# Optimization experiments

Hardware: AMD Instinct MI355X
Metric: run time of the kernel (lower is better)

## Reference

```python
import jax, jax.numpy as jnp
import numpy as np

EPS = 2e-05
N_H_RDG = 9   # lifting scale grid: h_j = 2**j, j=0..8
N_H_CROP = 3  # group-conv scale support: offsets 0,1,2 (dyadic index shifts)


def _scaled_kernel(w, h):
    """Resample base kernel w [O, I, K] (taps on integers centered at 0) at
    coordinates x/h via linear interpolation -> [O, I, (K-1)*h+1], with the
    R+ Haar-measure normalization 1/h (psi_h(x) = psi(x/h)/h)."""
    K = w.shape[-1]
    Kh = (K - 1) * h + 1
    m = jnp.arange(K, dtype=jnp.float32) - K // 2
    x = (jnp.arange(Kh, dtype=jnp.float32) - Kh // 2) / h
    hat = jnp.maximum(0.0, 1.0 - jnp.abs(x[:, None] - m[None, :]))  # [Kh, K]
    return jnp.einsum('oim,xm->oix', w, hat) / h


def _conv1d_same(x, k):
    pad = (k.shape[-1] - 1) // 2
    return jax.lax.conv_general_dilated(
        x, k, window_strides=(1,), padding=[(pad, pad)],
        dimension_numbers=('NCH', 'OIH', 'NCH'))


def _pool_r1(x, stride):
    # max pool over the spatial (last) axis only: kernel 4, pad 1 each side
    return jax.lax.reduce_window(
        x, -jnp.inf, jax.lax.max,
        window_dimensions=(1, 1, 1, 4), window_strides=(1, 1, 1, stride),
        padding=((0, 0), (0, 0), (0, 0), (1, 1)))


def _bn(x, g, b):
    # BatchNorm2d over [B, C, H_scale, L], training-mode batch stats
    mu = jnp.mean(x, axis=(0, 2, 3), keepdims=True)
    var = jnp.var(x, axis=(0, 2, 3), keepdims=True)
    return (x - mu) * jax.lax.rsqrt(var + EPS) * g[None, :, None, None] + b[None, :, None, None]


def _forward(x, w1, w2, w3, g1, b1, g2, b2, g3, b3, fw1, fb1, fw2, fb2, fw3, fb3):
    B = x.shape[0]
    # --- c1: GConvRdG lifting, scales h_j = 2**j, j=0..8 ---
    out = jnp.stack([_conv1d_same(x, _scaled_kernel(w1, 2 ** j))
                     for j in range(N_H_RDG)], axis=2)      # [B,16,9,16]
    out = _bn(jax.nn.relu(_pool_r1(out, 2)), g1, b1)        # [B,16,9,8]
    # --- c2: GConvGG, h_crop=True: out scale j uses in scales j..j+2 ---
    O2, I2 = w2.shape[0], w2.shape[1]
    w2r = w2.reshape(O2, I2 * N_H_CROP, 3)
    H2 = out.shape[2] - (N_H_CROP - 1)  # 7
    out = jnp.stack([
        _conv1d_same(out[:, :, j:j + N_H_CROP, :].reshape(B, I2 * N_H_CROP, -1),
                     _scaled_kernel(w2r, 2 ** j))
        for j in range(H2)], axis=2)                        # [B,32,7,8]
    out = _bn(jax.nn.relu(_pool_r1(out, 2)), g2, b2)        # [B,32,7,4]
    # --- c3: GConvGG with 1x1 spatial kernel ---
    w3s = w3[:, :, :, 0]  # [64,32,3]
    H3 = out.shape[2] - (N_H_CROP - 1)  # 5
    out = jnp.stack([
        jnp.einsum('oik,bikl->bol', w3s, out[:, :, j:j + N_H_CROP, :]) / (2.0 ** j)
        for j in range(H3)], axis=2)                        # [B,64,5,4]
    out = _bn(jax.nn.relu(_pool_r1(out, 4)), g3, b3)        # [B,64,5,1]
    # --- MLP head (dropout is identity in eval) ---
    out = out.reshape(B, -1)                                # [B,320]
    out = out @ fw1.T + fb1
    out = out @ fw2.T + fb2
    return out @ fw3.T + fb3                                # [B,17]


def setup_inputs() -> dict:
    key = jax.random.key(0)
    ks = jax.random.split(key, 7)
    B = 4096
    x = jax.random.normal(ks[0], (B, 6, 16), dtype=jnp.float32)
    w1 = jax.random.normal(ks[1], (16, 6, 7), dtype=jnp.float32) * (6 * 7) ** -0.5
    w2 = jax.random.normal(ks[2], (32, 16, 3, 3), dtype=jnp.float32) * (16 * 3 * 3) ** -0.5
    w3 = jax.random.normal(ks[3], (64, 32, 3, 1), dtype=jnp.float32) * (32 * 3) ** -0.5
    fw1 = jax.random.normal(ks[4], (16, 320), dtype=jnp.float32) * 320 ** -0.5
    fw2 = jax.random.normal(ks[5], (16, 16), dtype=jnp.float32) * 16 ** -0.5
    fw3 = jax.random.normal(ks[6], (17, 16), dtype=jnp.float32) * 16 ** -0.5
    return {
        'x': x, 'w1': w1, 'w2': w2, 'w3': w3,
        'g1': jnp.ones(16), 'b1': jnp.zeros(16),
        'g2': jnp.ones(32), 'b2': jnp.zeros(32),
        'g3': jnp.ones(64), 'b3': jnp.zeros(64),
        'fw1': fw1, 'fb1': jnp.zeros(16),
        'fw2': fw2, 'fb2': jnp.zeros(16),
        'fw3': fw3, 'fb3': jnp.zeros(17),
    }


def reference(x, w1, w2, w3, g1, b1, g2, b2, g3, b3, fw1, fb1, fw2, fb2, fw3, fb3):
    return _forward(x, w1, w2, w3, g1, b1, g2, b2, g3, b3, fw1, fb1, fw2, fb2, fw3, fb3)
```

## Files before the change

kernel.cpp:

```cpp
#include <hip/hip_runtime.h>

#define EPS 2e-5f

using short8  = __attribute__((ext_vector_type(8))) short;
using floatx4 = __attribute__((ext_vector_type(4))) float;

static __device__ inline unsigned short f2bf(float f) {
    unsigned u = __float_as_uint(f);
    u += 0x7fffu + ((u >> 16) & 1u);
    return (unsigned short)(u >> 16);
}


__global__ void __launch_bounds__(256) k_setup(const float* __restrict__ w1,
                                               unsigned short* __restrict__ W1f,
                                               float* __restrict__ stats) {
    int gid = blockIdx.x * 256 + threadIdx.x;
    if (gid < 256) stats[gid] = 0.f;
    if (gid >= 221184) return;
    int j  = gid / 24576;
    int r  = gid % 24576;
    int T  = r / 1536;
    int r2 = r % 1536;
    int ks = r2 / 512;
    int r3 = r2 % 512;
    int lane = r3 >> 3, e = r3 & 7;
    int n  = T * 16 + (lane & 15);
    int kk = ks * 32 + (lane >> 4) * 8 + e;
    int o = n >> 4, t = n & 15;
    int i = kk >> 4, s = kk & 15;
    int h = 1 << j;
    int d = s - t;
    float val = 0.f;
    if (d >= -3 * h && d <= 3 * h) {
        float df = (float)d / (float)h;
        #pragma unroll
        for (int m = 0; m < 7; ++m) {
            float hat = fmaxf(0.f, 1.f - fabsf(df - (float)(m - 3)));
            val += w1[(o * 6 + i) * 7 + m] * hat;
        }
        val /= (float)h;
    }
    W1f[gid] = f2bf(val);
}

__global__ void __launch_bounds__(256) k1(const float* __restrict__ x,
                                          const unsigned short* __restrict__ W1f,
                                          unsigned short* __restrict__ p1,
                                          float* __restrict__ stats1) {
    int j    = blockIdx.y;
    int wav  = threadIdx.x >> 6;
    int lane = threadIdx.x & 63;
    int msub = wav & 1, nh = wav >> 1;
    int mt   = blockIdx.x * 2 + msub;
    int quad = lane >> 4, l15 = lane & 15;
    floatx4 z = {0.f, 0.f, 0.f, 0.f};
    floatx4 acc[8];
    #pragma unroll
    for (int T = 0; T < 8; ++T) acc[T] = z;
    const float* xr = x + (size_t)(mt * 16 + l15) * 96;
    const short8* Bj = (const short8*)W1f + (size_t)(j * 16) * 3 * 64;
    #pragma unroll
    for (int ks = 0; ks < 3; ++ks) {
        int k0 = ks * 32 + quad * 8;
        floatx4 v0 = *(const floatx4*)(xr + k0);
        floatx4 v1 = *(const floatx4*)(xr + k0 + 4);
        short8 a;
        #pragma unroll
        for (int e = 0; e < 4; ++e) {
            a[e]     = (short)f2bf(v0[e]);
            a[e + 4] = (short)f2bf(v1[e]);
        }
        #pragma unroll
        for (int T = 0; T < 8; ++T) {
            short8 b = Bj[((nh * 8 + T) * 3 + ks) * 64 + lane];
            acc[T] = __builtin_amdgcn_mfma_f32_16x16x32_bf16(a, b, acc[T], 0, 0, 0);
        }
    }
    __shared__ float ls[32];
    if (threadIdx.x < 32) ls[threadIdx.x] = 0.f;
    __syncthreads();
    int mbase = mt * 16 + quad * 4;
    int tp = l15;
    bool act = tp < 8;
    int tpe = tp & 7;
    int base = lane & 48;
    int c0 = base + max(2 * tpe - 1, 0);
    int c1 = base + 2 * tpe;
    int c2 = base + 2 * tpe + 1;
    int c3 = base + min(2 * tpe + 2, 15);
    #pragma unroll
    for (int T = 0; T < 8; ++T) {
        int o = nh * 8 + T;
        float psum = 0.f, pss = 0.f;
        #pragma unroll
        for (int r = 0; r < 4; ++r) {
            float v  = acc[T][r];
            float mx = fmaxf(fmaxf(__shfl(v, c0, 64), __shfl(v, c1, 64)),
                             fmaxf(__shfl(v, c2, 64), __shfl(v, c3, 64)));
            mx = fmaxf(mx, 0.f);
            if (act) {
                p1[(size_t)(mbase + r) * 1152 + o * 72 + j * 8 + tp] = f2bf(mx);
                psum += mx; pss += mx * mx;
            }
        }
        #pragma unroll
        for (int m = 32; m >= 1; m >>= 1) {
            psum += __shfl_xor(psum, m, 64);
            pss  += __shfl_xor(pss,  m, 64);
        }
        if (lane == 0) {
            atomicAdd(&ls[o], psum);
            atomicAdd(&ls[16 + o], pss);
        }
    }
    __syncthreads();
    if (threadIdx.x < 16) {
        atomicAdd(&stats1[threadIdx.x], ls[threadIdx.x]);
        atomicAdd(&stats1[16 + threadIdx.x], ls[16 + threadIdx.x]);
    }
}

__global__ void __launch_bounds__(384) k_bias(const float* __restrict__ w2,
                                              const float* __restrict__ g1,
                                              const float* __restrict__ b1,
                                              const float* __restrict__ stats1,
                                              unsigned short* __restrict__ W2f,
                                              float* __restrict__ bias2,
                                              float invN1) {
    int blk = blockIdx.x;
    int j   = blk >> 8;
    int col = blk & 255;
    int o = col >> 3, t = col & 7;
    int k = threadIdx.x;
    int ic = k >> 3, s = k & 7;
    int i = ic / 3, c = ic % 3;
    float mu  = stats1[i] * invN1;
    float var = stats1[16 + i] * invN1 - mu * mu;
    float rsg = rsqrtf(var + EPS);
    float a1  = g1[i] * rsg;
    float d1  = b1[i] - mu * a1;
    int h = 1 << j;
    int d = s - t;
    float raw = 0.f;
    if (d >= -h && d <= h) {
        float df = (float)d / (float)h;
        #pragma unroll
        for (int m = 0; m < 3; ++m) {
            float hat = fmaxf(0.f, 1.f - fabsf(df - (float)(m - 1)));
            raw += w2[((o * 16 + i) * 3 + c) * 3 + m] * hat;
        }
        raw /= (float)h;
    }
    {
        int T    = col >> 4;
        int lane = (col & 15) + ((k >> 3) & 3) * 16;
        int ks   = k >> 5;
        int e    = k & 7;
        W2f[(((size_t)(j * 16 + T) * 12 + ks) * 64 + lane) * 8 + e] = f2bf(raw * a1);
    }
    __shared__ float red[384];
    red[k] = raw * d1;
    __syncthreads();
    if (k < 128) red[k] += red[k + 128] + red[k + 256];
    __syncthreads();
    for (int st = 64; st >= 1; st >>= 1) {
        if (k < st) red[k] += red[k + st];
        __syncthreads();
    }
    if (k == 0) bias2[j * 256 + col] = red[0];
}

__global__ void __launch_bounds__(256) k2(const unsigned short* __restrict__ p1,
                                          const unsigned short* __restrict__ W2f,
                                          const float* __restrict__ bias2,
                                          unsigned short* __restrict__ p2s,
                                          float* __restrict__ stats2,
                                          int B) {
    int j    = blockIdx.y;
    int wav  = threadIdx.x >> 6;
    int lane = threadIdx.x & 63;
    int nh   = wav & 1, mp = wav >> 1;
    int m0   = blockIdx.x * 64 + mp * 32;
    int quad = lane >> 4, l15 = lane & 15;
    floatx4 z = {0.f, 0.f, 0.f, 0.f};
    floatx4 acc[2][8];
    #pragma unroll
    for (int mi = 0; mi < 2; ++mi)
        #pragma unroll
        for (int T = 0; T < 8; ++T) acc[mi][T] = z;
    const short8* Bj = (const short8*)W2f + (size_t)(j * 16) * 12 * 64;
    const unsigned short* Arow0 = p1 + (size_t)(m0 + l15) * 1152;
    const unsigned short* Arow1 = Arow0 + 16 * 1152;
    #pragma unroll
    for (int ks = 0; ks < 12; ++ks) {
        int k0 = ks * 32 + quad * 8;
        int i  = k0 / 24;
        int c  = (k0 - i * 24) >> 3;
        int off = i * 72 + (j + c) * 8;
        short8 a0 = *(const short8*)(Arow0 + off);
        short8 a1 = *(const short8*)(Arow1 + off);
        #pragma unroll
        for (int T = 0; T < 8; ++T) {
            short8 b = Bj[((nh * 8 + T) * 12 + ks) * 64 + lane];
            acc[0][T] = __builtin_amdgcn_mfma_f32_16x16x32_bf16(a0, b, acc[0][T], 0, 0, 0);
            acc[1][T] = __builtin_amdgcn_mfma_f32_16x16x32_bf16(a1, b, acc[1][T], 0, 0, 0);
        }
    }
    __shared__ float ls[64];
    if (threadIdx.x < 64) ls[threadIdx.x] = 0.f;
    __syncthreads();
    int tp  = lane & 7;
    bool act = tp < 4;
    int tpe = tp & 3;
    int base = lane & 56;
    int c0 = base + max(2 * tpe - 1, 0);
    int c1 = base + 2 * tpe;
    int c2 = base + 2 * tpe + 1;
    int c3 = base + min(2 * tpe + 2, 7);
    #pragma unroll
    for (int T = 0; T < 8; ++T) {
        int n = (nh * 8 + T) * 16 + l15;
        int o = n >> 3;
        float bias = bias2[j * 256 + n];
        float psum = 0.f, pss = 0.f;
        #pragma unroll
        for (int mi = 0; mi < 2; ++mi) {
            int mbase = m0 + mi * 16 + quad * 4;
            #pragma unroll
            for (int r = 0; r < 4; ++r) {
                float v  = acc[mi][T][r] + bias;
                float mx = fmaxf(fmaxf(__shfl(v, c0, 64), __shfl(v, c1, 64)),
                                 fmaxf(__shfl(v, c2, 64), __shfl(v, c3, 64)));
                mx = fmaxf(mx, 0.f);
                if (act) {
                    p2s[(((size_t)j * 4 + tp) * B + mbase + r) * 32 + o] = f2bf(mx);
                    psum += mx; pss += mx * mx;
                }
            }
        }
        #pragma unroll
        for (int m = 0; m < 5; ++m) {
            int msk = (m < 3) ? (1 << m) : (1 << (m + 1));
            psum += __shfl_xor(psum, msk, 64);
            pss  += __shfl_xor(pss,  msk, 64);
        }
        if (lane == 0 || lane == 8) {
            int oo = (nh * 8 + T) * 2 + (lane >> 3);
            atomicAdd(&ls[oo], psum);
            atomicAdd(&ls[32 + oo], pss);
        }
    }
    __syncthreads();
    if (threadIdx.x < 32) {
        atomicAdd(&stats2[threadIdx.x], ls[threadIdx.x]);
        atomicAdd(&stats2[32 + threadIdx.x], ls[32 + threadIdx.x]);
    }
}

__global__ void __launch_bounds__(256) k3(const unsigned short* __restrict__ p2s,
                                          const float* __restrict__ w3,
                                          const float* __restrict__ g2,
                                          const float* __restrict__ b2,
                                          const float* __restrict__ stats2,
                                          float* __restrict__ act3,
                                          float* __restrict__ stats3,
                                          float invN2, int B) {
    int j    = blockIdx.y;
    int wav  = threadIdx.x >> 6;
    int lane = threadIdx.x & 63;
    int msub = wav & 1, nh = wav >> 1;
    int m0   = (blockIdx.x * 2 + msub) * 16;
    int quad = lane >> 4, l15 = lane & 15;
    __shared__ float a2s[32], d2s[32], bias3s[64], ls[128];
    __shared__ unsigned short W3s[6144];
    if (threadIdx.x < 128) ls[threadIdx.x] = 0.f;
    if (threadIdx.x < 32) {
        int i = threadIdx.x;
        float mu  = stats2[i] * invN2;
        float var = stats2[32 + i] * invN2 - mu * mu;
        float rsg = rsqrtf(var + EPS);
        a2s[i] = g2[i] * rsg;
        d2s[i] = b2[i] - mu * a2s[i];
    }
    __syncthreads();
    for (int idx = threadIdx.x; idx < 6144; idx += 256) {
        int e  = idx & 7;
        int ln = (idx >> 3) & 63;
        int fs = idx >> 9;
        int Tg = fs / 3, ks = fs % 3;
        int n = Tg * 16 + (ln & 15);
        int i = (ln >> 4) * 8 + e;
        W3s[idx] = f2bf(w3[n * 96 + i * 3 + ks] * a2s[i]);
    }
    if (threadIdx.x < 64) {
        float s = 0.f;
        for (int i = 0; i < 32; ++i)
            #pragma unroll
            for (int kk = 0; kk < 3; ++kk)
                s = fmaf(w3[threadIdx.x * 96 + i * 3 + kk], d2s[i], s);
        bias3s[threadIdx.x] = s;
    }
    __syncthreads();
    short8 bf[2][3];
    #pragma unroll
    for (int T = 0; T < 2; ++T)
        #pragma unroll
        for (int ks = 0; ks < 3; ++ks)
            bf[T][ks] = *(const short8*)&W3s[(((nh * 2 + T) * 3 + ks) * 64 + lane) * 8];
    floatx4 z = {0.f, 0.f, 0.f, 0.f};
    floatx4 acc[2][3];
    #pragma unroll
    for (int T = 0; T < 2; ++T)
        #pragma unroll
        for (int l = 0; l < 3; ++l) acc[T][l] = z;
    #pragma unroll
    for (int ks = 0; ks < 3; ++ks) {
        int jj = j + ks;
        #pragma unroll
        for (int l = 0; l < 3; ++l) {
            const short8* ap =
                (const short8*)(p2s + ((size_t)(jj * 4 + l) * B + m0 + l15) * 32) + quad;
            short8 a = *ap;
            #pragma unroll
            for (int T = 0; T < 2; ++T)
                acc[T][l] = __builtin_amdgcn_mfma_f32_16x16x32_bf16(a, bf[T][ks],
                                                                    acc[T][l], 0, 0, 0);
        }
    }
    float inv = 1.f / (float)(1 << j);
    int mbase = m0 + quad * 4;
    #pragma unroll
    for (int T = 0; T < 2; ++T) {
        int col = nh * 32 + T * 16 + l15;
        float bias = bias3s[col];
        float psum = 0.f, pss = 0.f;
        #pragma unroll
        for (int r = 0; r < 4; ++r) {
            float v = fmaxf(fmaxf(acc[T][0][r], acc[T][1][r]), acc[T][2][r]);
            v = fmaxf((v + bias) * inv, 0.f);
            act3[(size_t)(mbase + r) * 320 + col * 5 + j] = v;
            psum += v; pss += v * v;
        }
        psum += __shfl_xor(psum, 16, 64); pss += __shfl_xor(pss, 16, 64);
        psum += __shfl_xor(psum, 32, 64); pss += __shfl_xor(pss, 32, 64);
        if (quad == 0) {
            atomicAdd(&ls[col], psum);
            atomicAdd(&ls[64 + col], pss);
        }
    }
    __syncthreads();
    if (threadIdx.x < 64) {
        atomicAdd(&stats3[threadIdx.x], ls[threadIdx.x]);
        atomicAdd(&stats3[64 + threadIdx.x], ls[64 + threadIdx.x]);
    }
}

__global__ void __launch_bounds__(128) k4(const float* __restrict__ act3,
                                          const float* __restrict__ g3,
                                          const float* __restrict__ b3,
                                          const float* __restrict__ stats3,
                                          const float* __restrict__ fw1,
                                          const float* __restrict__ fb1,
                                          const float* __restrict__ fw2,
                                          const float* __restrict__ fb2,
                                          const float* __restrict__ fw3,
                                          const float* __restrict__ fb3,
                                          float* __restrict__ out,
                                          float invN3) {
    __shared__ float a3s[64], d3s[64];
    __shared__ unsigned short W1s[5120];
    __shared__ float fw2s[256], fw3s[272], fb2s[16], fb3s[17], fb1f[16];
    __shared__ float hbuf[2][16][17];
    int tid = threadIdx.x;
    if (tid < 64) {
        float mu  = stats3[tid] * invN3;
        float var = stats3[64 + tid] * invN3 - mu * mu;
        float rsg = rsqrtf(var + EPS);
        a3s[tid] = g3[tid] * rsg;
        d3s[tid] = b3[tid] - mu * a3s[tid];
    }
    __syncthreads();
    for (int idx = tid; idx < 5120; idx += 128) {
        int e  = idx & 7;
        int ln = (idx >> 3) & 63;
        int ks = idx >> 9;
        int n  = ln & 15;
        int k  = ks * 32 + (ln >> 4) * 8 + e;
        W1s[idx] = f2bf(fw1[n * 320 + k] * a3s[k / 5]);
    }
    for (int idx = tid; idx < 256; idx += 128) fw2s[idx] = fw2[idx];
    for (int idx = tid; idx < 272; idx += 128) fw3s[idx] = fw3[idx];
    if (tid < 16) fb2s[tid] = fb2[tid];
    if (tid < 17) fb3s[tid] = fb3[tid];
    if (tid < 16) {
        float s = fb1[tid];
        for (int o = 0; o < 64; ++o) {
            float dd = d3s[o];
            #pragma unroll
            for (int jj = 0; jj < 5; ++jj)
                s = fmaf(fw1[tid * 320 + o * 5 + jj], dd, s);
        }
        fb1f[tid] = s;
    }
    __syncthreads();
    int wav = tid >> 6, lane = tid & 63;
    int quad = lane >> 4, l15 = lane & 15;
    int mt = blockIdx.x * 2 + wav;
    const float* ar = act3 + (size_t)(mt * 16 + l15) * 320;
    floatx4 acc = {0.f, 0.f, 0.f, 0.f};
    #pragma unroll
    for (int ks = 0; ks < 10; ++ks) {
        int k0 = ks * 32 + quad * 8;
        floatx4 v0 = *(const floatx4*)(ar + k0);
        floatx4 v1 = *(const floatx4*)(ar + k0 + 4);
        short8 a;
        #pragma unroll
        for (int e = 0; e < 4; ++e) {
            a[e]     = (short)f2bf(v0[e]);
            a[e + 4] = (short)f2bf(v1[e]);
        }
        short8 b = *(const short8*)&W1s[(ks * 64 + lane) * 8];
        acc = __builtin_amdgcn_mfma_f32_16x16x32_bf16(a, b, acc, 0, 0, 0);
    }
    #pragma unroll
    for (int r = 0; r < 4; ++r)
        hbuf[wav][quad * 4 + r][l15] = acc[r] + fb1f[l15];
    __syncthreads();
    if (lane < 16) {
        int row = l15;
        float hv[16];
        #pragma unroll
        for (int n = 0; n < 16; ++n) hv[n] = hbuf[wav][row][n];
        float h2[16];
        #pragma unroll
        for (int f2 = 0; f2 < 16; ++f2) {
            float s = fb2s[f2];
            #pragma unroll
            for (int n = 0; n < 16; ++n) s = fmaf(fw2s[f2 * 16 + n], hv[n], s);
            h2[f2] = s;
        }
        float* orow = out + (size_t)(mt * 16 + row) * 17;
        #pragma unroll
        for (int f3 = 0; f3 < 17; ++f3) {
            float s = fb3s[f3];
            #pragma unroll
            for (int n = 0; n < 16; ++n) s = fmaf(fw3s[f3 * 16 + n], h2[n], s);
            orow[f3] = s;
        }
    }
}

extern "C" void kernel_launch(void* const* d_in, const int* in_sizes, int n_in,
                              void* d_out, int out_size, void* d_ws, size_t ws_size,
                              hipStream_t stream) {
    (void)n_in; (void)out_size; (void)ws_size;
    const float* x   = (const float*)d_in[0];
    const float* w1  = (const float*)d_in[1];
    const float* w2  = (const float*)d_in[2];
    const float* w3  = (const float*)d_in[3];
    const float* g1  = (const float*)d_in[4];
    const float* b1  = (const float*)d_in[5];
    const float* g2  = (const float*)d_in[6];
    const float* b2  = (const float*)d_in[7];
    const float* g3  = (const float*)d_in[8];
    const float* b3  = (const float*)d_in[9];
    const float* fw1 = (const float*)d_in[10];
    const float* fb1 = (const float*)d_in[11];
    const float* fw2 = (const float*)d_in[12];
    const float* fb2 = (const float*)d_in[13];
    const float* fw3 = (const float*)d_in[14];
    const float* fb3 = (const float*)d_in[15];
    float* out = (float*)d_out;

    int B = in_sizes[0] / 96;

    char* wsb = (char*)d_ws;
    float*          stats  = (float*)wsb;
    unsigned short* W1f    = (unsigned short*)(wsb + 1024);
    unsigned short* W2f    = W1f + 221184;
    float*          bias2  = (float*)(W2f + 688128);
    unsigned short* p1     = (unsigned short*)(bias2 + 1792);
    unsigned short* p2s    = p1 + (size_t)B * 1152;
    float*          act3   = (float*)(p2s + (size_t)B * 896);

    float* stats1 = stats;
    float* stats2 = stats + 32;
    float* stats3 = stats + 96;

    float invN1 = 1.f / (float)(B * 72);
    float invN2 = 1.f / (float)(B * 28);
    float invN3 = 1.f / (float)(B * 5);

    k_setup<<<864, 256, 0, stream>>>(w1, W1f, stats);
    k1<<<dim3(B / 32, 9), 256, 0, stream>>>(x, W1f, p1, stats1);
    k_bias<<<7 * 256, 384, 0, stream>>>(w2, g1, b1, stats1, W2f, bias2, invN1);
    k2<<<dim3(B / 64, 7), 256, 0, stream>>>(p1, W2f, bias2, p2s, stats2, B);
    k3<<<dim3(B / 32, 5), 256, 0, stream>>>(p2s, w3, g2, b2, stats2, act3, stats3,
                                            invN2, B);
    k4<<<B / 32, 128, 0, stream>>>(act3, g3, b3, stats3, fw1, fb1, fw2, fb2, fw3, fb3,
                                   out, invN3);
}
```

Baseline: 204.1 us.

## Fuse weight prep into conv kernels, use per-block stat partials and bf16 activations

Removes the separate weight-setup and bias kernels: each conv kernel now builds its scaled bf16 weight fragments in registers from the raw weights and folds the BN affine of the previous layer in-kernel. Global atomics for batch statistics are replaced by per-block partial sums reduced by the consumer kernel. Intermediate layouts are changed to scale-major and act3 is stored as bf16, and grids are made persistent-ish with fixed block counts looping over tiles. This cuts kernel launches, workspace traffic and atomic contention, at the cost of redundant weight recomputation per block and a smaller, hardcoded grid (e.g. 32 blocks in x) that ties work split to B=4096.

```diff
diff --git a/kernel.cpp b/kernel.cpp
--- a/kernel.cpp
+++ b/kernel.cpp
@@ -3,6 +3,7 @@
 #define EPS 2e-5f
 
 using short8  = __attribute__((ext_vector_type(8))) short;
+using short4v = __attribute__((ext_vector_type(4))) short;
 using floatx4 = __attribute__((ext_vector_type(4))) float;
 
 static __device__ inline unsigned short f2bf(float f) {
@@ -12,75 +13,49 @@
 }
 
 
-__global__ void __launch_bounds__(256) k_setup(const float* __restrict__ w1,
-                                               unsigned short* __restrict__ W1f,
-                                               float* __restrict__ stats) {
-    int gid = blockIdx.x * 256 + threadIdx.x;
-    if (gid < 256) stats[gid] = 0.f;
-    if (gid >= 221184) return;
-    int j  = gid / 24576;
-    int r  = gid % 24576;
-    int T  = r / 1536;
-    int r2 = r % 1536;
-    int ks = r2 / 512;
-    int r3 = r2 % 512;
-    int lane = r3 >> 3, e = r3 & 7;
-    int n  = T * 16 + (lane & 15);
-    int kk = ks * 32 + (lane >> 4) * 8 + e;
-    int o = n >> 4, t = n & 15;
-    int i = kk >> 4, s = kk & 15;
+__global__ void __launch_bounds__(256) k1(const float* __restrict__ x,
+                                          const float* __restrict__ w1,
+                                          unsigned short* __restrict__ p1,
+                                          float* __restrict__ partials1,
+                                          int B) {
+    __shared__ float w1s[672];
+    __shared__ float ls[32];
+    __shared__ unsigned short ptile[32][16][8];
+    int tid = threadIdx.x, j = blockIdx.y;
+    int wav = tid >> 6, lane = tid & 63;
+    int quad = lane >> 4, l15 = lane & 15;
+    int msub = wav & 1, nh = wav >> 1;
+    for (int idx = tid; idx < 672; idx += 256) w1s[idx] = w1[idx];
+    if (tid < 32) ls[tid] = 0.f;
+    __syncthreads();
     int h = 1 << j;
-    int d = s - t;
-    float val = 0.f;
-    if (d >= -3 * h && d <= 3 * h) {
-        float df = (float)d / (float)h;
-        #pragma unroll
-        for (int m = 0; m < 7; ++m) {
-            float hat = fmaxf(0.f, 1.f - fabsf(df - (float)(m - 3)));
-            val += w1[(o * 6 + i) * 7 + m] * hat;
-        }
-        val /= (float)h;
-    }
-    W1f[gid] = f2bf(val);
-}
-
-__global__ void __launch_bounds__(256) k1(const float* __restrict__ x,
-                                          const unsigned short* __restrict__ W1f,
-                                          unsigned short* __restrict__ p1,
-                                          float* __restrict__ stats1) {
-    int j    = blockIdx.y;
-    int wav  = threadIdx.x >> 6;
-    int lane = threadIdx.x & 63;
-    int msub = wav & 1, nh = wav >> 1;
-    int mt   = blockIdx.x * 2 + msub;
-    int quad = lane >> 4, l15 = lane & 15;
-    floatx4 z = {0.f, 0.f, 0.f, 0.f};
-    floatx4 acc[8];
-    #pragma unroll
-    for (int T = 0; T < 8; ++T) acc[T] = z;
-    const float* xr = x + (size_t)(mt * 16 + l15) * 96;
-    const short8* Bj = (const short8*)W1f + (size_t)(j * 16) * 3 * 64;
-    #pragma unroll
-    for (int ks = 0; ks < 3; ++ks) {
-        int k0 = ks * 32 + quad * 8;
-        floatx4 v0 = *(const floatx4*)(xr + k0);
-        floatx4 v1 = *(const floatx4*)(xr + k0 + 4);
-        short8 a;
-        #pragma unroll
-        for (int e = 0; e < 4; ++e) {
-            a[e]     = (short)f2bf(v0[e]);
-            a[e + 4] = (short)f2bf(v1[e]);
-        }
-        #pragma unroll
-        for (int T = 0; T < 8; ++T) {
-            short8 b = Bj[((nh * 8 + T) * 3 + ks) * 64 + lane];
-            acc[T] = __builtin_amdgcn_mfma_f32_16x16x32_bf16(a, b, acc[T], 0, 0, 0);
-        }
-    }
-    __shared__ float ls[32];
-    if (threadIdx.x < 32) ls[threadIdx.x] = 0.f;
-    __syncthreads();
-    int mbase = mt * 16 + quad * 4;
+    float hInv = 1.f / (float)h;
+    short8 bf[8][3];
+    #pragma unroll
+    for (int T = 0; T < 8; ++T) {
+        int o = nh * 8 + T;
+        #pragma unroll
+        for (int ks = 0; ks < 3; ++ks) {
+            short8 v;
+            #pragma unroll
+            for (int e = 0; e < 8; ++e) {
+                int k = ks * 32 + quad * 8 + e;
+                int i = k >> 4, s = k & 15;
+                int d = s - l15;
+                float val = 0.f;
+                if (d >= -3 * h && d <= 3 * h) {
+                    float u = (float)d * hInv + 3.f;
+                    int m0 = (int)u;
+                    float f = u - (float)m0;
+                    int m1 = min(m0 + 1, 6);
+                    const float* wr = &w1s[(o * 6 + i) * 7];
+                    val = (wr[m0] * (1.f - f) + wr[m1] * f) * hInv;
+                }
+                v[e] = (short)f2bf(val);
+            }
+            bf[T][ks] = v;
+        }
+    }
     int tp = l15;
     bool act = tp < 8;
     int tpe = tp & 7;
@@ -89,277 +64,317 @@
     int c1 = base + 2 * tpe;
     int c2 = base + 2 * tpe + 1;
     int c3 = base + min(2 * tpe + 2, 15);
-    #pragma unroll
-    for (int T = 0; T < 8; ++T) {
-        int o = nh * 8 + T;
-        float psum = 0.f, pss = 0.f;
-        #pragma unroll
-        for (int r = 0; r < 4; ++r) {
-            float v  = acc[T][r];
-            float mx = fmaxf(fmaxf(__shfl(v, c0, 64), __shfl(v, c1, 64)),
-                             fmaxf(__shfl(v, c2, 64), __shfl(v, c3, 64)));
-            mx = fmaxf(mx, 0.f);
-            if (act) {
-                p1[(size_t)(mbase + r) * 1152 + o * 72 + j * 8 + tp] = f2bf(mx);
-                psum += mx; pss += mx * mx;
-            }
-        }
-        #pragma unroll
-        for (int m = 32; m >= 1; m >>= 1) {
-            psum += __shfl_xor(psum, m, 64);
-            pss  += __shfl_xor(pss,  m, 64);
-        }
-        if (lane == 0) {
-            atomicAdd(&ls[o], psum);
-            atomicAdd(&ls[16 + o], pss);
-        }
-    }
-    __syncthreads();
-    if (threadIdx.x < 16) {
-        atomicAdd(&stats1[threadIdx.x], ls[threadIdx.x]);
-        atomicAdd(&stats1[16 + threadIdx.x], ls[16 + threadIdx.x]);
-    }
-}
-
-__global__ void __launch_bounds__(384) k_bias(const float* __restrict__ w2,
-                                              const float* __restrict__ g1,
-                                              const float* __restrict__ b1,
-                                              const float* __restrict__ stats1,
-                                              unsigned short* __restrict__ W2f,
-                                              float* __restrict__ bias2,
-                                              float invN1) {
-    int blk = blockIdx.x;
-    int j   = blk >> 8;
-    int col = blk & 255;
-    int o = col >> 3, t = col & 7;
-    int k = threadIdx.x;
-    int ic = k >> 3, s = k & 7;
-    int i = ic / 3, c = ic % 3;
-    float mu  = stats1[i] * invN1;
-    float var = stats1[16 + i] * invN1 - mu * mu;
-    float rsg = rsqrtf(var + EPS);
-    float a1  = g1[i] * rsg;
-    float d1  = b1[i] - mu * a1;
-    int h = 1 << j;
-    int d = s - t;
-    float raw = 0.f;
-    if (d >= -h && d <= h) {
-        float df = (float)d / (float)h;
-        #pragma unroll
-        for (int m = 0; m < 3; ++m) {
-            float hat = fmaxf(0.f, 1.f - fabsf(df - (float)(m - 1)));
-            raw += w2[((o * 16 + i) * 3 + c) * 3 + m] * hat;
-        }
-        raw /= (float)h;
-    }
-    {
-        int T    = col >> 4;
-        int lane = (col & 15) + ((k >> 3) & 3) * 16;
-        int ks   = k >> 5;
-        int e    = k & 7;
-        W2f[(((size_t)(j * 16 + T) * 12 + ks) * 64 + lane) * 8 + e] = f2bf(raw * a1);
-    }
-    __shared__ float red[384];
-    red[k] = raw * d1;
-    __syncthreads();
-    if (k < 128) red[k] += red[k + 128] + red[k + 256];
-    __syncthreads();
-    for (int st = 64; st >= 1; st >>= 1) {
-        if (k < st) red[k] += red[k + st];
+    for (int it = 0; it < 4; ++it) {
+        int t32 = blockIdx.x * 4 + it;
+        int mt  = t32 * 2 + msub;
+        floatx4 z = {0.f, 0.f, 0.f, 0.f};
+        floatx4 acc[8];
+        #pragma unroll
+        for (int T = 0; T < 8; ++T) acc[T] = z;
+        const float* xr = x + (size_t)(mt * 16 + l15) * 96;
+        #pragma unroll
+        for (int ks = 0; ks < 3; ++ks) {
+            int k0 = ks * 32 + quad * 8;
+            floatx4 v0 = *(const floatx4*)(xr + k0);
+            floatx4 v1 = *(const floatx4*)(xr + k0 + 4);
+            short8 a;
+            #pragma unroll
+            for (int e = 0; e < 4; ++e) {
+                a[e]     = (short)f2bf(v0[e]);
+                a[e + 4] = (short)f2bf(v1[e]);
+            }
+            #pragma unroll
+            for (int T = 0; T < 8; ++T)
+                acc[T] = __builtin_amdgcn_mfma_f32_16x16x32_bf16(a, bf[T][ks], acc[T], 0, 0, 0);
+        }
         __syncthreads();
-    }
-    if (k == 0) bias2[j * 256 + col] = red[0];
-}
-
-__global__ void __launch_bounds__(256) k2(const unsigned short* __restrict__ p1,
-                                          const unsigned short* __restrict__ W2f,
-                                          const float* __restrict__ bias2,
-                                          unsigned short* __restrict__ p2s,
-                                          float* __restrict__ stats2,
-                                          int B) {
-    int j    = blockIdx.y;
-    int wav  = threadIdx.x >> 6;
-    int lane = threadIdx.x & 63;
-    int nh   = wav & 1, mp = wav >> 1;
-    int m0   = blockIdx.x * 64 + mp * 32;
-    int quad = lane >> 4, l15 = lane & 15;
-    floatx4 z = {0.f, 0.f, 0.f, 0.f};
-    floatx4 acc[2][8];
-    #pragma unroll
-    for (int mi = 0; mi < 2; ++mi)
-        #pragma unroll
-        for (int T = 0; T < 8; ++T) acc[mi][T] = z;
-    const short8* Bj = (const short8*)W2f + (size_t)(j * 16) * 12 * 64;
-    const unsigned short* Arow0 = p1 + (size_t)(m0 + l15) * 1152;
-    const unsigned short* Arow1 = Arow0 + 16 * 1152;
-    #pragma unroll
-    for (int ks = 0; ks < 12; ++ks) {
-        int k0 = ks * 32 + quad * 8;
-        int i  = k0 / 24;
-        int c  = (k0 - i * 24) >> 3;
-        int off = i * 72 + (j + c) * 8;
-        short8 a0 = *(const short8*)(Arow0 + off);
-        short8 a1 = *(const short8*)(Arow1 + off);
+        int row_l = msub * 16 + quad * 4;
         #pragma unroll
         for (int T = 0; T < 8; ++T) {
-            short8 b = Bj[((nh * 8 + T) * 12 + ks) * 64 + lane];
-            acc[0][T] = __builtin_amdgcn_mfma_f32_16x16x32_bf16(a0, b, acc[0][T], 0, 0, 0);
-            acc[1][T] = __builtin_amdgcn_mfma_f32_16x16x32_bf16(a1, b, acc[1][T], 0, 0, 0);
-        }
-    }
-    __shared__ float ls[64];
-    if (threadIdx.x < 64) ls[threadIdx.x] = 0.f;
-    __syncthreads();
-    int tp  = lane & 7;
-    bool act = tp < 4;
-    int tpe = tp & 3;
-    int base = lane & 56;
-    int c0 = base + max(2 * tpe - 1, 0);
-    int c1 = base + 2 * tpe;
-    int c2 = base + 2 * tpe + 1;
-    int c3 = base + min(2 * tpe + 2, 7);
-    #pragma unroll
-    for (int T = 0; T < 8; ++T) {
-        int n = (nh * 8 + T) * 16 + l15;
-        int o = n >> 3;
-        float bias = bias2[j * 256 + n];
-        float psum = 0.f, pss = 0.f;
-        #pragma unroll
-        for (int mi = 0; mi < 2; ++mi) {
-            int mbase = m0 + mi * 16 + quad * 4;
+            int o = nh * 8 + T;
+            float psum = 0.f, pss = 0.f;
             #pragma unroll
             for (int r = 0; r < 4; ++r) {
-                float v  = acc[mi][T][r] + bias;
+                float v  = acc[T][r];
                 float mx = fmaxf(fmaxf(__shfl(v, c0, 64), __shfl(v, c1, 64)),
                                  fmaxf(__shfl(v, c2, 64), __shfl(v, c3, 64)));
                 mx = fmaxf(mx, 0.f);
                 if (act) {
-                    p2s[(((size_t)j * 4 + tp) * B + mbase + r) * 32 + o] = f2bf(mx);
+                    ptile[row_l + r][o][tp] = f2bf(mx);
                     psum += mx; pss += mx * mx;
                 }
             }
-        }
-        #pragma unroll
-        for (int m = 0; m < 5; ++m) {
-            int msk = (m < 3) ? (1 << m) : (1 << (m + 1));
-            psum += __shfl_xor(psum, msk, 64);
-            pss  += __shfl_xor(pss,  msk, 64);
-        }
-        if (lane == 0 || lane == 8) {
-            int oo = (nh * 8 + T) * 2 + (lane >> 3);
-            atomicAdd(&ls[oo], psum);
-            atomicAdd(&ls[32 + oo], pss);
-        }
-    }
-    __syncthreads();
-    if (threadIdx.x < 32) {
-        atomicAdd(&stats2[threadIdx.x], ls[threadIdx.x]);
-        atomicAdd(&stats2[32 + threadIdx.x], ls[32 + threadIdx.x]);
-    }
+            #pragma unroll
+            for (int m = 32; m >= 1; m >>= 1) {
+                psum += __shfl_xor(psum, m, 64);
+                pss  += __shfl_xor(pss,  m, 64);
+            }
+            if (lane == 0) {
+                atomicAdd(&ls[o], psum);
+                atomicAdd(&ls[16 + o], pss);
+            }
+        }
+        __syncthreads();
+        unsigned short* dst = p1 + ((size_t)j * B + t32 * 32) * 128;
+        #pragma unroll
+        for (int u = 0; u < 2; ++u) {
+            int c = tid + u * 256;
+            int rr = c >> 4, oo = c & 15;
+            *(short8*)(dst + (size_t)rr * 128 + oo * 8) = *(const short8*)&ptile[rr][oo][0];
+        }
+    }
+    __syncthreads();
+    if (tid < 32) partials1[(size_t)(blockIdx.y * 32 + blockIdx.x) * 32 + tid] = ls[tid];
+}
+
+__global__ void __launch_bounds__(256) k2(const unsigned short* __restrict__ p1,
+                                          const float* __restrict__ w2,
+                                          const float* __restrict__ g1,
+                                          const float* __restrict__ b1,
+                                          const float* __restrict__ partials1,
+                                          unsigned short* __restrict__ p2s,
+                                          float* __restrict__ partials2,
+                                          int B) {
+    __shared__ float w2s[4608];
+    __shared__ float red[8][32];
+    __shared__ float st1[32];
+    __shared__ float a1s[16], d1s[16];
+    __shared__ float wt[4][2][16][17];
+    __shared__ float wbias[4][16];
+    __shared__ unsigned short pt[4 * 32 * 8];
+    __shared__ float ls2[64];
+    int tid = threadIdx.x;
+    int w = tid >> 6, lane = tid & 63;
+    int quad = lane >> 4, l15 = lane & 15;
+    int j = blockIdx.z, cs = blockIdx.y;
+    float invN1 = 1.f / (float)(B * 72);
+    for (int idx = tid; idx < 4608; idx += 256) w2s[idx] = w2[idx];
+    {
+        int ch = tid & 31, grp = tid >> 5;
+        float s = 0.f;
+        for (int g = grp; g < 288; g += 8) s += partials1[(size_t)g * 32 + ch];
+        red[grp][ch] = s;
+    }
+    if (tid < 64) ls2[tid] = 0.f;
+    __syncthreads();
+    if (tid < 32) {
+        float s = 0.f;
+        #pragma unroll
+        for (int g = 0; g < 8; ++g) s += red[g][tid];
+        st1[tid] = s;
+    }
+    __syncthreads();
+    if (tid < 16) {
+        float mu  = st1[tid] * invN1;
+        float var = st1[16 + tid] * invN1 - mu * mu;
+        float rs  = rsqrtf(var + EPS);
+        a1s[tid] = g1[tid] * rs;
+        d1s[tid] = b1[tid] - mu * a1s[tid];
+    }
+    __syncthreads();
+    int h = 1 << j;
+    float hInv = 1.f / (float)h;
+    int n = cs * 64 + w * 16 + l15;
+    int o = n >> 3, t = n & 7;
+    float biasacc = 0.f;
+    short8 af[12];
+    #pragma unroll
+    for (int ks = 0; ks < 12; ++ks) {
+        int ic = ks * 4 + quad;
+        int i = ic / 3, c = ic - i * 3;
+        const float* wr = &w2s[((o * 16 + i) * 3 + c) * 3];
+        short8 v;
+        #pragma unroll
+        for (int e = 0; e < 8; ++e) {
+            int d = e - t;
+            float raw = 0.f;
+            if (d >= -h && d <= h) {
+                float u = (float)d * hInv + 1.f;
+                int m0 = (int)u;
+                float f = u - (float)m0;
+                int m1 = min(m0 + 1, 2);
+                raw = (wr[m0] * (1.f - f) + wr[m1] * f) * hInv;
+            }
+            v[e] = (short)f2bf(raw * a1s[i]);
+            biasacc = fmaf(raw, d1s[i], biasacc);
+        }
+        af[ks] = v;
+    }
+    biasacc += __shfl_xor(biasacc, 16, 64);
+    biasacc += __shfl_xor(biasacc, 32, 64);
+    if (quad == 0) wbias[w][l15] = biasacc;
+    __syncthreads();
+    float ps[2] = {0.f, 0.f}, pq[2] = {0.f, 0.f};
+    int lo = max(0, 2 * quad - 1), hi = min(7, 2 * quad + 2);
+    for (int it = 0; it < 8; ++it) {
+        int b0 = (blockIdx.x * 16 + it * 2) * 16;
+        floatx4 accA = {0.f, 0.f, 0.f, 0.f};
+        floatx4 accB = {0.f, 0.f, 0.f, 0.f};
+        #pragma unroll
+        for (int ks = 0; ks < 12; ++ks) {
+            int ic = ks * 4 + quad;
+            int i = ic / 3, c = ic - i * 3;
+            const unsigned short* pr = p1 + ((size_t)(j + c) * B + b0 + l15) * 128 + i * 8;
+            short8 bA = *(const short8*)pr;
+            short8 bB = *(const short8*)(pr + 16 * 128);
+            accA = __builtin_amdgcn_mfma_f32_16x16x32_bf16(af[ks], bA, accA, 0, 0, 0);
+            accB = __builtin_amdgcn_mfma_f32_16x16x32_bf16(af[ks], bB, accB, 0, 0, 0);
+        }
+        __syncthreads();
+        #pragma unroll
+        for (int r = 0; r < 4; ++r) {
+            float br = wbias[w][quad * 4 + r];
+            wt[w][0][quad * 4 + r][l15] = accA[r] + br;
+            wt[w][1][quad * 4 + r][l15] = accB[r] + br;
+        }
+        __syncthreads();
+        #pragma unroll
+        for (int s_ = 0; s_ < 2; ++s_)
+            #pragma unroll
+            for (int u = 0; u < 2; ++u) {
+                float m = -1e30f;
+                for (int t_ = lo; t_ <= hi; ++t_) m = fmaxf(m, wt[w][s_][u * 8 + t_][l15]);
+                float v = fmaxf(m, 0.f);
+                pt[(quad * 32 + s_ * 16 + l15) * 8 + w * 2 + u] = f2bf(v);
+                ps[u] += v; pq[u] += v * v;
+            }
+        __syncthreads();
+        {
+            int tpp = tid >> 6, rem = tid & 63;
+            int bL = rem >> 1, og = rem & 1;
+            *(short4v*)(p2s + ((size_t)(j * 4 + tpp) * B + b0 + bL) * 32 + cs * 8 + og * 4) =
+                *(const short4v*)&pt[(tpp * 32 + bL) * 8 + og * 4];
+        }
+    }
+    #pragma unroll
+    for (int m = 1; m <= 32; m <<= 1) {
+        #pragma unroll
+        for (int u = 0; u < 2; ++u) {
+            ps[u] += __shfl_xor(ps[u], m, 64);
+            pq[u] += __shfl_xor(pq[u], m, 64);
+        }
+    }
+    if (lane == 0) {
+        int o0 = cs * 8 + w * 2;
+        #pragma unroll
+        for (int u = 0; u < 2; ++u) {
+            ls2[(o0 + u) * 2]     = ps[u];
+            ls2[(o0 + u) * 2 + 1] = pq[u];
+        }
+    }
+    __syncthreads();
+    int bid = blockIdx.x + 16 * (cs + 4 * j);
+    if (tid < 64) partials2[(size_t)bid * 64 + tid] = ls2[tid];
 }
 
 __global__ void __launch_bounds__(256) k3(const unsigned short* __restrict__ p2s,
                                           const float* __restrict__ w3,
                                           const float* __restrict__ g2,
                                           const float* __restrict__ b2,
-                                          const float* __restrict__ stats2,
-                                          float* __restrict__ act3,
-                                          float* __restrict__ stats3,
-                                          float invN2, int B) {
-    int j    = blockIdx.y;
-    int wav  = threadIdx.x >> 6;
-    int lane = threadIdx.x & 63;
-    int msub = wav & 1, nh = wav >> 1;
-    int m0   = (blockIdx.x * 2 + msub) * 16;
+                                          const float* __restrict__ partials2,
+                                          unsigned short* __restrict__ act3,
+                                          float* __restrict__ partials3,
+                                          int B) {
+    __shared__ float w3s[6144];
+    __shared__ float red[4][64];
+    __shared__ float st2[64];
+    __shared__ float a2s[32], d2s[32];
+    __shared__ float ls3[128];
+    int tid = threadIdx.x;
+    int wav = tid >> 6, lane = tid & 63;
     int quad = lane >> 4, l15 = lane & 15;
-    __shared__ float a2s[32], d2s[32], bias3s[64], ls[128];
-    __shared__ unsigned short W3s[6144];
-    if (threadIdx.x < 128) ls[threadIdx.x] = 0.f;
-    if (threadIdx.x < 32) {
-        int i = threadIdx.x;
-        float mu  = stats2[i] * invN2;
-        float var = stats2[32 + i] * invN2 - mu * mu;
-        float rsg = rsqrtf(var + EPS);
-        a2s[i] = g2[i] * rsg;
-        d2s[i] = b2[i] - mu * a2s[i];
-    }
-    __syncthreads();
-    for (int idx = threadIdx.x; idx < 6144; idx += 256) {
-        int e  = idx & 7;
-        int ln = (idx >> 3) & 63;
-        int fs = idx >> 9;
-        int Tg = fs / 3, ks = fs % 3;
-        int n = Tg * 16 + (ln & 15);
-        int i = (ln >> 4) * 8 + e;
-        W3s[idx] = f2bf(w3[n * 96 + i * 3 + ks] * a2s[i]);
-    }
-    if (threadIdx.x < 64) {
+    int j = blockIdx.y;
+    float invN2 = 1.f / (float)(B * 28);
+    for (int idx = tid; idx < 6144; idx += 256) w3s[idx] = w3[idx];
+    {
+        int ch = tid & 63, grp = tid >> 6;
         float s = 0.f;
-        for (int i = 0; i < 32; ++i)
-            #pragma unroll
-            for (int kk = 0; kk < 3; ++kk)
-                s = fmaf(w3[threadIdx.x * 96 + i * 3 + kk], d2s[i], s);
-        bias3s[threadIdx.x] = s;
-    }
-    __syncthreads();
-    short8 bf[2][3];
-    #pragma unroll
-    for (int T = 0; T < 2; ++T)
-        #pragma unroll
-        for (int ks = 0; ks < 3; ++ks)
-            bf[T][ks] = *(const short8*)&W3s[(((nh * 2 + T) * 3 + ks) * 64 + lane) * 8];
-    floatx4 z = {0.f, 0.f, 0.f, 0.f};
-    floatx4 acc[2][3];
-    #pragma unroll
-    for (int T = 0; T < 2; ++T)
-        #pragma unroll
-        for (int l = 0; l < 3; ++l) acc[T][l] = z;
-    #pragma unroll
-    for (int ks = 0; ks < 3; ++ks) {
-        int jj = j + ks;
-        #pragma unroll
-        for (int l = 0; l < 3; ++l) {
-            const short8* ap =
-                (const short8*)(p2s + ((size_t)(jj * 4 + l) * B + m0 + l15) * 32) + quad;
-            short8 a = *ap;
-            #pragma unroll
-            for (int T = 0; T < 2; ++T)
-                acc[T][l] = __builtin_amdgcn_mfma_f32_16x16x32_bf16(a, bf[T][ks],
-                                                                    acc[T][l], 0, 0, 0);
-        }
-    }
+        for (int g = grp; g < 448; g += 4) s += partials2[(size_t)g * 64 + ch];
+        red[grp][ch] = s;
+    }
+    __syncthreads();
+    if (tid < 64) st2[tid] = red[0][tid] + red[1][tid] + red[2][tid] + red[3][tid];
+    __syncthreads();
+    if (tid < 32) {
+        float mu  = st2[tid * 2] * invN2;
+        float var = st2[tid * 2 + 1] * invN2 - mu * mu;
+        float rs  = rsqrtf(var + EPS);
+        a2s[tid] = g2[tid] * rs;
+        d2s[tid] = b2[tid] - mu * a2s[tid];
+    }
+    __syncthreads();
+    int og = wav;
+    int o  = og * 16 + l15;
+    float biasacc = 0.f;
+    short8 af[3];
+    #pragma unroll
+    for (int kf = 0; kf < 3; ++kf) {
+        short8 v;
+        #pragma unroll
+        for (int e = 0; e < 8; ++e) {
+            int i = quad * 8 + e;
+            float raw = w3s[o * 96 + i * 3 + kf];
+            v[e] = (short)f2bf(raw * a2s[i]);
+            biasacc = fmaf(raw, d2s[i], biasacc);
+        }
+        af[kf] = v;
+    }
+    biasacc += __shfl_xor(biasacc, 16, 64);
+    biasacc += __shfl_xor(biasacc, 32, 64);
+    float brow[4];
+    #pragma unroll
+    for (int r = 0; r < 4; ++r) brow[r] = __shfl(biasacc, quad * 4 + r, 64);
     float inv = 1.f / (float)(1 << j);
-    int mbase = m0 + quad * 4;
-    #pragma unroll
-    for (int T = 0; T < 2; ++T) {
-        int col = nh * 32 + T * 16 + l15;
-        float bias = bias3s[col];
-        float psum = 0.f, pss = 0.f;
+    float ps[4] = {0.f, 0.f, 0.f, 0.f}, pq[4] = {0.f, 0.f, 0.f, 0.f};
+    for (int it = 0; it < 8; ++it) {
+        int b0 = (blockIdx.x * 8 + it) * 16;
+        floatx4 aL0 = {0.f, 0.f, 0.f, 0.f};
+        floatx4 aL1 = {0.f, 0.f, 0.f, 0.f};
+        floatx4 aL2 = {0.f, 0.f, 0.f, 0.f};
+        #pragma unroll
+        for (int c = 0; c < 3; ++c) {
+            const unsigned short* prb = p2s + ((size_t)(j + c) * 4 * B + b0 + l15) * 32 + quad * 8;
+            short8 b0f = *(const short8*)prb;
+            short8 b1f = *(const short8*)(prb + (size_t)B * 32);
+            short8 b2f = *(const short8*)(prb + (size_t)2 * B * 32);
+            aL0 = __builtin_amdgcn_mfma_f32_16x16x32_bf16(af[c], b0f, aL0, 0, 0, 0);
+            aL1 = __builtin_amdgcn_mfma_f32_16x16x32_bf16(af[c], b1f, aL1, 0, 0, 0);
+            aL2 = __builtin_amdgcn_mfma_f32_16x16x32_bf16(af[c], b2f, aL2, 0, 0, 0);
+        }
+        short4v pk;
         #pragma unroll
         for (int r = 0; r < 4; ++r) {
-            float v = fmaxf(fmaxf(acc[T][0][r], acc[T][1][r]), acc[T][2][r]);
-            v = fmaxf((v + bias) * inv, 0.f);
-            act3[(size_t)(mbase + r) * 320 + col * 5 + j] = v;
-            psum += v; pss += v * v;
-        }
-        psum += __shfl_xor(psum, 16, 64); pss += __shfl_xor(pss, 16, 64);
-        psum += __shfl_xor(psum, 32, 64); pss += __shfl_xor(pss, 32, 64);
-        if (quad == 0) {
-            atomicAdd(&ls[col], psum);
-            atomicAdd(&ls[64 + col], pss);
-        }
-    }
-    __syncthreads();
-    if (threadIdx.x < 64) {
-        atomicAdd(&stats3[threadIdx.x], ls[threadIdx.x]);
-        atomicAdd(&stats3[64 + threadIdx.x], ls[64 + threadIdx.x]);
-    }
+            float vm = fmaxf(fmaxf(aL0[r], aL1[r]), aL2[r]);
+            float v  = fmaxf((vm + brow[r]) * inv, 0.f);
+            pk[r] = (short)f2bf(v);
+            ps[r] += v; pq[r] += v * v;
+        }
+        *(short4v*)(act3 + ((size_t)j * B + b0 + l15) * 64 + og * 16 + quad * 4) = pk;
+    }
+    #pragma unroll
+    for (int m = 1; m <= 8; m <<= 1) {
+        #pragma unroll
+        for (int r = 0; r < 4; ++r) {
+            ps[r] += __shfl_xor(ps[r], m, 64);
+            pq[r] += __shfl_xor(pq[r], m, 64);
+        }
+    }
+    if (l15 == 0) {
+        #pragma unroll
+        for (int r = 0; r < 4; ++r) {
+            ls3[(og * 16 + quad * 4 + r) * 2]     = ps[r];
+            ls3[(og * 16 + quad * 4 + r) * 2 + 1] = pq[r];
+        }
+    }
+    __syncthreads();
+    int bid = blockIdx.x + 32 * j;
+    if (tid < 128) partials3[(size_t)bid * 128 + tid] = ls3[tid];
 }
 
-__global__ void __launch_bounds__(128) k4(const float* __restrict__ act3,
+__global__ void __launch_bounds__(256) k4(const unsigned short* __restrict__ act3,
                                           const float* __restrict__ g3,
                                           const float* __restrict__ b3,
-                                          const float* __restrict__ stats3,
+                                          const float* __restrict__ partials3,
                                           const float* __restrict__ fw1,
                                           const float* __restrict__ fb1,
                                           const float* __restrict__ fw2,
@@ -367,62 +382,70 @@
                                           const float* __restrict__ fw3,
                                           const float* __restrict__ fb3,
                                           float* __restrict__ out,
-                                          float invN3) {
+                                          int B) {
+    __shared__ float red[2][128];
+    __shared__ float st3[128];
     __shared__ float a3s[64], d3s[64];
     __shared__ unsigned short W1s[5120];
     __shared__ float fw2s[256], fw3s[272], fb2s[16], fb3s[17], fb1f[16];
-    __shared__ float hbuf[2][16][17];
+    __shared__ float hbuf[4][16][17];
     int tid = threadIdx.x;
+    int wav = tid >> 6, lane = tid & 63;
+    int quad = lane >> 4, l15 = lane & 15;
+    float invN3 = 1.f / (float)(B * 5);
+    {
+        int ch = tid & 127, grp = tid >> 7;
+        float s = 0.f;
+        for (int g = grp; g < 160; g += 2) s += partials3[(size_t)g * 128 + ch];
+        red[grp][ch] = s;
+    }
+    __syncthreads();
+    if (tid < 128) st3[tid] = red[0][tid] + red[1][tid];
+    __syncthreads();
     if (tid < 64) {
-        float mu  = stats3[tid] * invN3;
-        float var = stats3[64 + tid] * invN3 - mu * mu;
-        float rsg = rsqrtf(var + EPS);
-        a3s[tid] = g3[tid] * rsg;
+        float mu  = st3[tid * 2] * invN3;
+        float var = st3[tid * 2 + 1] * invN3 - mu * mu;
+        float rs  = rsqrtf(var + EPS);
+        a3s[tid] = g3[tid] * rs;
         d3s[tid] = b3[tid] - mu * a3s[tid];
     }
     __syncthreads();
-    for (int idx = tid; idx < 5120; idx += 128) {
+    for (int idx = tid; idx < 5120; idx += 256) {
         int e  = idx & 7;
         int ln = (idx >> 3) & 63;
-        int ks = idx >> 9;
-        int n  = ln & 15;
-        int k  = ks * 32 + (ln >> 4) * 8 + e;
-        W1s[idx] = f2bf(fw1[n * 320 + k] * a3s[k / 5]);
-    }
-    for (int idx = tid; idx < 256; idx += 128) fw2s[idx] = fw2[idx];
-    for (int idx = tid; idx < 272; idx += 128) fw3s[idx] = fw3[idx];
+        int fs = idx >> 9;
+        int jj = fs >> 1, ks = fs & 1;
+        int n = ln & 15;
+        int o = ks * 32 + (ln >> 4) * 8 + e;
+        W1s[idx] = f2bf(fw1[n * 320 + o * 5 + jj] * a3s[o]);
+    }
+    if (tid < 256) fw2s[tid] = fw2[tid];
+    for (int idx = tid; idx < 272; idx += 256) fw3s[idx] = fw3[idx];
     if (tid < 16) fb2s[tid] = fb2[tid];
     if (tid < 17) fb3s[tid] = fb3[tid];
-    if (tid < 16) {
-        float s = fb1[tid];
+    if (tid >= 32 && tid < 48) {
+        int f = tid - 32;
+        float s = fb1[f];
         for (int o = 0; o < 64; ++o) {
             float dd = d3s[o];
             #pragma unroll
             for (int jj = 0; jj < 5; ++jj)
-                s = fmaf(fw1[tid * 320 + o * 5 + jj], dd, s);
-        }
-        fb1f[tid] = s;
-    }
-    __syncthreads();
-    int wav = tid >> 6, lane = tid & 63;
-    int quad = lane >> 4, l15 = lane & 15;
-    int mt = blockIdx.x * 2 + wav;
-    const float* ar = act3 + (size_t)(mt * 16 + l15) * 320;
+                s = fmaf(fw1[f * 320 + o * 5 + jj], dd, s);
+        }
+        fb1f[f] = s;
+    }
+    __syncthreads();
+    int mt = blockIdx.x * 4 + wav;
     floatx4 acc = {0.f, 0.f, 0.f, 0.f};
     #pragma unroll
-    for (int ks = 0; ks < 10; ++ks) {
-        int k0 = ks * 32 + quad * 8;
-        floatx4 v0 = *(const floatx4*)(ar + k0);
-        floatx4 v1 = *(const floatx4*)(ar + k0 + 4);
-        short8 a;
-        #pragma unroll
-        for (int e = 0; e < 4; ++e) {
-            a[e]     = (short)f2bf(v0[e]);
-            a[e + 4] = (short)f2bf(v1[e]);
-        }
-        short8 b = *(const short8*)&W1s[(ks * 64 + lane) * 8];
-        acc = __builtin_amdgcn_mfma_f32_16x16x32_bf16(a, b, acc, 0, 0, 0);
-    }
+    for (int jj = 0; jj < 5; ++jj)
+        #pragma unroll
+        for (int ks = 0; ks < 2; ++ks) {
+            short8 a = *(const short8*)(act3 +
+                ((size_t)jj * B + mt * 16 + l15) * 64 + ks * 32 + quad * 8);
+            short8 b = *(const short8*)&W1s[((jj * 2 + ks) * 64 + lane) * 8];
+            acc = __builtin_amdgcn_mfma_f32_16x16x32_bf16(a, b, acc, 0, 0, 0);
+        }
     #pragma unroll
     for (int r = 0; r < 4; ++r)
         hbuf[wav][quad * 4 + r][l15] = acc[r] + fb1f[l15];
@@ -476,28 +499,16 @@
     int B = in_sizes[0] / 96;
 
     char* wsb = (char*)d_ws;
-    float*          stats  = (float*)wsb;
-    unsigned short* W1f    = (unsigned short*)(wsb + 1024);
-    unsigned short* W2f    = W1f + 221184;
-    float*          bias2  = (float*)(W2f + 688128);
-    unsigned short* p1     = (unsigned short*)(bias2 + 1792);
-    unsigned short* p2s    = p1 + (size_t)B * 1152;
-    float*          act3   = (float*)(p2s + (size_t)B * 896);
-
-    float* stats1 = stats;
-    float* stats2 = stats + 32;
-    float* stats3 = stats + 96;
-
-    float invN1 = 1.f / (float)(B * 72);
-    float invN2 = 1.f / (float)(B * 28);
-    float invN3 = 1.f / (float)(B * 5);
-
-    k_setup<<<864, 256, 0, stream>>>(w1, W1f, stats);
-    k1<<<dim3(B / 32, 9), 256, 0, stream>>>(x, W1f, p1, stats1);
-    k_bias<<<7 * 256, 384, 0, stream>>>(w2, g1, b1, stats1, W2f, bias2, invN1);
-    k2<<<dim3(B / 64, 7), 256, 0, stream>>>(p1, W2f, bias2, p2s, stats2, B);
-    k3<<<dim3(B / 32, 5), 256, 0, stream>>>(p2s, w3, g2, b2, stats2, act3, stats3,
-                                            invN2, B);
-    k4<<<B / 32, 128, 0, stream>>>(act3, g3, b3, stats3, fw1, fb1, fw2, fb2, fw3, fb3,
-                                   out, invN3);
+    float* partials1 = (float*)wsb;
+    float* partials2 = partials1 + 288 * 32;
+    float* partials3 = partials2 + 448 * 64;
+    unsigned short* p1   = (unsigned short*)(partials3 + 160 * 128);
+    unsigned short* p2s  = p1 + (size_t)9 * B * 128;
+    unsigned short* act3 = p2s + (size_t)28 * B * 32;
+
+    k1<<<dim3(32, 9), 256, 0, stream>>>(x, w1, p1, partials1, B);
+    k2<<<dim3(16, 4, 7), 256, 0, stream>>>(p1, w2, g1, b1, partials1, p2s, partials2, B);
+    k3<<<dim3(32, 5), 256, 0, stream>>>(p2s, w3, g2, b2, partials2, act3, partials3, B);
+    k4<<<B / 64, 256, 0, stream>>>(act3, g3, b3, partials3, fw1, fb1, fw2, fb2, fw3, fb3,
+                                   out, B);
 }
```

New measurement: 296.2 us. 45.1% more time.
